# Optimization experiments

Hardware: AMD Instinct MI355X
Metric: run time of the kernel (lower is better)

Reference implementation:

```python
import jax, jax.numpy as jnp
import numpy as np

HIDDEN = 128
IN = 28
OUT = 28


def _uniform(key, shape, fan_in):
    bound = 1.0 / np.sqrt(fan_in)
    return jax.random.uniform(key, shape, jnp.float32, -bound, bound)


def setup_inputs() -> dict:
    key = jax.random.key(0)
    ks = jax.random.split(key, 8)
    B, T = 4096, 256
    x = jax.random.normal(ks[0], (B, T, IN), jnp.float32)
    hidden = jnp.zeros((B, HIDDEN), jnp.float32)
    # torch nn.Linear default init: U(-1/sqrt(fan_in), 1/sqrt(fan_in))
    W_ih = _uniform(ks[1], (HIDDEN, IN), IN)
    b_ih = _uniform(ks[2], (HIDDEN,), IN)
    W_hh = _uniform(ks[3], (HIDDEN, HIDDEN), HIDDEN)
    b_hh = _uniform(ks[4], (HIDDEN,), HIDDEN)
    W_ho = _uniform(ks[5], (OUT * OUT, HIDDEN), HIDDEN)
    b_ho = _uniform(ks[6], (OUT * OUT,), HIDDEN)
    return {"x": x, "hidden": hidden, "W_ih": W_ih, "b_ih": b_ih,
            "W_hh": W_hh, "b_hh": b_hh, "W_ho": W_ho, "b_ho": b_ho}


def reference(x, hidden, W_ih, b_ih, W_hh, b_hh, W_ho, b_ho):
    # x: [B, T, IN]; hidden: [B, HIDDEN]
    def step(h, x_t):
        h = jax.nn.relu(x_t @ W_ih.T + b_ih + h @ W_hh.T + b_hh)
        return h, None

    # scan over time (leading axis) — equivalent to the python loop,
    # and only the final hidden feeds the output projection (the torch
    # code overwrites `output` every step, so only the last one matters).
    h_final, _ = jax.lax.scan(step, hidden, jnp.swapaxes(x, 0, 1))
    out = (h_final @ W_ho.T + b_ho).reshape(-1, OUT, OUT)  # [B, 28, 28]
    return out, h_final
```

## Files before the change

kernel.cpp:

```cpp
#include <hip/hip_runtime.h>
#include <hip/hip_bf16.h>

#define B_TOT   4096
#define T_STEPS 256
#define IN_D    28
#define HID     128
#define OUT_D   784
#define BM      16

typedef __bf16 bf16x8 __attribute__((ext_vector_type(8)));
typedef __bf16 bf16x4 __attribute__((ext_vector_type(4)));
typedef float  f32x4  __attribute__((ext_vector_type(4)));
typedef float  f32x2  __attribute__((ext_vector_type(2)));

__device__ __forceinline__ float bf2f(__bf16 b) {
    unsigned short s = __builtin_bit_cast(unsigned short, b);
    unsigned int u = ((unsigned int)s) << 16;
    return __builtin_bit_cast(float, u);
}
__device__ __forceinline__ unsigned short f2bfbits(float f) {
    unsigned int u = __builtin_bit_cast(unsigned int, f);
    u += 0x7fffu + ((u >> 16) & 1u);
    return (unsigned short)(u >> 16);
}

__device__ __forceinline__ int hswz(int row, int byteInRow) {
    return row * 256 + (byteInRow ^ ((row & 7) << 4));
}

__global__ __launch_bounds__(256) void rnn_fused(
    const float* __restrict__ x,
    const float* __restrict__ h0,
    const float* __restrict__ W_ih,
    const float* __restrict__ b_ih,
    const float* __restrict__ W_hh,
    const float* __restrict__ b_hh,
    const float* __restrict__ W_ho,
    const float* __restrict__ b_ho,
    float* __restrict__ out)
{
    __shared__ __align__(16) unsigned char Hb[2][BM * 256];
    __shared__ __align__(16) unsigned char Xb[2][BM * 80];

    const int tid  = threadIdx.x;
    const int lane = tid & 63;
    const int wv   = tid >> 6;
    const int ln15 = lane & 15;
    const int lg   = lane >> 4;
    const int b0   = blockIdx.x * BM;

    const int nt0 = wv * 32;
    bf16x8 bw[2][4];
    #pragma unroll
    for (int ti = 0; ti < 2; ++ti) {
        int n = nt0 + ti * 16 + ln15;
        #pragma unroll
        for (int kc = 0; kc < 4; ++kc) {
            const float* p = W_hh + n * HID + kc * 32 + lg * 8;
            bf16x8 v;
            #pragma unroll
            for (int e = 0; e < 8; ++e) v[e] = (__bf16)p[e];
            bw[ti][kc] = v;
        }
    }
    const __bf16 bzero = (__bf16)0.0f;
    bf16x8 bxf[2];
    #pragma unroll
    for (int ti = 0; ti < 2; ++ti) {
        int n = nt0 + ti * 16 + ln15;
        bf16x8 v;
        #pragma unroll
        for (int e = 0; e < 8; ++e) {
            int k = lg * 8 + e;
            v[e] = (k < IN_D) ? (__bf16)W_ih[n * IN_D + k] : bzero;
        }
        bxf[ti] = v;
    }
    f32x4 bias4[2];
    #pragma unroll
    for (int ti = 0; ti < 2; ++ti) {
        int n = nt0 + ti * 16 + 4 * lg;
        f32x4 bi = *(const f32x4*)(b_ih + n);
        f32x4 bh = *(const f32x4*)(b_hh + n);
        bias4[ti] = bi + bh;
    }

    {
        int row = tid >> 4, cg = tid & 15;
        const float* p = h0 + (size_t)(b0 + row) * HID + cg * 8;
        bf16x8 hv;
        #pragma unroll
        for (int e = 0; e < 8; ++e) hv[e] = (__bf16)p[e];
        *(bf16x8*)(&Hb[0][hswz(row, cg * 16)]) = hv;
    }
    if (tid < 64) {
        int bufi = tid >> 5, idx = tid & 31, row = idx >> 1, half = idx & 1;
        *(unsigned int*)(&Xb[bufi][row * 80 + 56 + half * 4]) = 0u;
    }
    const int xrow = tid / 14, xpair = tid % 14;
    const bool xthr = (tid < 224);
    const float* xbase = x + (size_t)(b0 + xrow) * T_STEPS * IN_D + xpair * 2;
    if (xthr) {
        f32x2 v = *(const f32x2*)(xbase + 0 * IN_D);
        unsigned int pk = ((unsigned int)f2bfbits(v[1]) << 16) | f2bfbits(v[0]);
        *(unsigned int*)(&Xb[0][xrow * 80 + xpair * 4]) = pk;
    }
    f32x2 p0 = {0.f, 0.f}, p1 = p0, p2 = p0, p3 = p0;
    if (xthr) {
        p0 = *(const f32x2*)(xbase + 1 * IN_D);
        p1 = *(const f32x2*)(xbase + 2 * IN_D);
        p2 = *(const f32x2*)(xbase + 3 * IN_D);
        p3 = *(const f32x2*)(xbase + 4 * IN_D);
    }
    __syncthreads();

#define STEP(T, P)                                                              \
    {                                                                           \
        const int rb = (T) & 1;                                                 \
        bf16x8 ax  = *(const bf16x8*)(&Xb[rb][ln15 * 80 + lg * 16]);            \
        bf16x8 ah0 = *(const bf16x8*)(&Hb[rb][hswz(ln15,   0 + lg * 16)]);      \
        bf16x8 ah1 = *(const bf16x8*)(&Hb[rb][hswz(ln15,  64 + lg * 16)]);      \
        bf16x8 ah2 = *(const bf16x8*)(&Hb[rb][hswz(ln15, 128 + lg * 16)]);      \
        bf16x8 ah3 = *(const bf16x8*)(&Hb[rb][hswz(ln15, 192 + lg * 16)]);      \
        if (((T) + 1 < T_STEPS) && xthr) {                                      \
            unsigned int pk = ((unsigned int)f2bfbits(P[1]) << 16) | f2bfbits(P[0]); \
            *(unsigned int*)(&Xb[rb ^ 1][xrow * 80 + xpair * 4]) = pk;          \
        }                                                                       \
        if (((T) + 5 < T_STEPS) && xthr)                                        \
            P = *(const f32x2*)(xbase + (size_t)((T) + 5) * IN_D);              \
        f32x4 a0 = bias4[0], a1 = bias4[1];                                     \
        f32x4 c0 = {0.f, 0.f, 0.f, 0.f}, c1 = c0;                               \
        a0 = __builtin_amdgcn_mfma_f32_16x16x32_bf16(bxf[0],   ax,  a0, 0, 0, 0); \
        a1 = __builtin_amdgcn_mfma_f32_16x16x32_bf16(bxf[1],   ax,  a1, 0, 0, 0); \
        a0 = __builtin_amdgcn_mfma_f32_16x16x32_bf16(bw[0][0], ah0, a0, 0, 0, 0); \
        a1 = __builtin_amdgcn_mfma_f32_16x16x32_bf16(bw[1][0], ah0, a1, 0, 0, 0); \
        c0 = __builtin_amdgcn_mfma_f32_16x16x32_bf16(bw[0][1], ah1, c0, 0, 0, 0); \
        c1 = __builtin_amdgcn_mfma_f32_16x16x32_bf16(bw[1][1], ah1, c1, 0, 0, 0); \
        a0 = __builtin_amdgcn_mfma_f32_16x16x32_bf16(bw[0][2], ah2, a0, 0, 0, 0); \
        a1 = __builtin_amdgcn_mfma_f32_16x16x32_bf16(bw[1][2], ah2, a1, 0, 0, 0); \
        c0 = __builtin_amdgcn_mfma_f32_16x16x32_bf16(bw[0][3], ah3, c0, 0, 0, 0); \
        c1 = __builtin_amdgcn_mfma_f32_16x16x32_bf16(bw[1][3], ah3, c1, 0, 0, 0); \
        _Pragma("unroll")                                                       \
        for (int ti = 0; ti < 2; ++ti) {                                        \
            f32x4 s = ti ? (a1 + c1) : (a0 + c0);                               \
            bf16x4 w;                                                           \
            _Pragma("unroll")                                                   \
            for (int r = 0; r < 4; ++r) {                                       \
                float v = s[r];                                                 \
                w[r] = (__bf16)(v > 0.f ? v : 0.f);                             \
            }                                                                   \
            *(bf16x4*)(&Hb[rb ^ 1][hswz(ln15, nt0 * 2 + ti * 32 + lg * 8)]) = w; \
        }                                                                       \
        __syncthreads();                                                        \
    }

    for (int t = 0; t < T_STEPS; t += 4) {
        STEP(t + 0, p0)
        STEP(t + 1, p1)
        STEP(t + 2, p2)
        STEP(t + 3, p3)
    }
#undef STEP

    {
        int row = tid >> 4, cg = tid & 15;
        bf16x8 hv = *(const bf16x8*)(&Hb[0][hswz(row, cg * 16)]);
        float* po = out + (size_t)B_TOT * OUT_D + (size_t)(b0 + row) * HID + cg * 8;
        #pragma unroll
        for (int e = 0; e < 8; ++e) po[e] = bf2f(hv[e]);
    }
    bf16x8 af[4];
    #pragma unroll
    for (int kc = 0; kc < 4; ++kc)
        af[kc] = *(const bf16x8*)(&Hb[0][hswz(ln15, kc * 64 + lg * 16)]);

    for (int nt = wv; nt < 49; nt += 4) {
        f32x4 acc = *(const f32x4*)(b_ho + nt * 16 + 4 * lg);
        #pragma unroll
        for (int kc = 0; kc < 4; ++kc) {
            const float* p = W_ho + (nt * 16 + ln15) * HID + kc * 32 + lg * 8;
            bf16x8 bfrag;
            #pragma unroll
            for (int e = 0; e < 8; ++e) bfrag[e] = (__bf16)p[e];
            acc = __builtin_amdgcn_mfma_f32_16x16x32_bf16(bfrag, af[kc], acc, 0, 0, 0);
        }
        *(f32x4*)(out + (size_t)(b0 + ln15) * OUT_D + nt * 16 + 4 * lg) = acc;
    }
}

extern "C" void kernel_launch(void* const* d_in, const int* in_sizes, int n_in,
                              void* d_out, int out_size, void* d_ws, size_t ws_size,
                              hipStream_t stream) {
    const float* x    = (const float*)d_in[0];
    const float* h0   = (const float*)d_in[1];
    const float* W_ih = (const float*)d_in[2];
    const float* b_ih = (const float*)d_in[3];
    const float* W_hh = (const float*)d_in[4];
    const float* b_hh = (const float*)d_in[5];
    const float* W_ho = (const float*)d_in[6];
    const float* b_ho = (const float*)d_in[7];
    rnn_fused<<<B_TOT / BM, 256, 0, stream>>>(x, h0, W_ih, b_ih, W_hh, b_hh,
                                              W_ho, b_ho, (float*)d_out);
}
```

Measured before the change: 105.2 us.

## Load x fragments straight into registers and use an LDS-only barrier

Drops the shared-memory staging buffer for the input sequence. Each lane now loads its own MFMA x operand from global memory four steps ahead and converts it to bf16 in registers, so the per-step LDS write and read of x go away. Every wave issues its own x loads instead of sharing one staged copy, which adds redundant global loads. `__syncthreads` is replaced by a custom barrier that waits only on LDS counters, so outstanding global prefetches no longer stall the per-step barrier. This relies on the hand-written waitcnt being sufficient for correctness.

```diff
diff --git a/kernel.cpp b/kernel.cpp
--- a/kernel.cpp
+++ b/kernel.cpp
@@ -11,22 +11,18 @@
 typedef __bf16 bf16x8 __attribute__((ext_vector_type(8)));
 typedef __bf16 bf16x4 __attribute__((ext_vector_type(4)));
 typedef float  f32x4  __attribute__((ext_vector_type(4)));
-typedef float  f32x2  __attribute__((ext_vector_type(2)));
 
 __device__ __forceinline__ float bf2f(__bf16 b) {
     unsigned short s = __builtin_bit_cast(unsigned short, b);
     unsigned int u = ((unsigned int)s) << 16;
     return __builtin_bit_cast(float, u);
 }
-__device__ __forceinline__ unsigned short f2bfbits(float f) {
-    unsigned int u = __builtin_bit_cast(unsigned int, f);
-    u += 0x7fffu + ((u >> 16) & 1u);
-    return (unsigned short)(u >> 16);
-}
 
 __device__ __forceinline__ int hswz(int row, int byteInRow) {
     return row * 256 + (byteInRow ^ ((row & 7) << 4));
 }
+
+#define BAR() asm volatile("s_waitcnt lgkmcnt(0)\n\ts_barrier" ::: "memory")
 
 __global__ __launch_bounds__(256) void rnn_fused(
     const float* __restrict__ x,
@@ -40,7 +36,6 @@
     float* __restrict__ out)
 {
     __shared__ __align__(16) unsigned char Hb[2][BM * 256];
-    __shared__ __align__(16) unsigned char Xb[2][BM * 80];
 
     const int tid  = threadIdx.x;
     const int lane = tid & 63;
@@ -93,49 +88,37 @@
         for (int e = 0; e < 8; ++e) hv[e] = (__bf16)p[e];
         *(bf16x8*)(&Hb[0][hswz(row, cg * 16)]) = hv;
     }
-    if (tid < 64) {
-        int bufi = tid >> 5, idx = tid & 31, row = idx >> 1, half = idx & 1;
-        *(unsigned int*)(&Xb[bufi][row * 80 + 56 + half * 4]) = 0u;
-    }
-    const int xrow = tid / 14, xpair = tid % 14;
-    const bool xthr = (tid < 224);
-    const float* xbase = x + (size_t)(b0 + xrow) * T_STEPS * IN_D + xpair * 2;
-    if (xthr) {
-        f32x2 v = *(const f32x2*)(xbase + 0 * IN_D);
-        unsigned int pk = ((unsigned int)f2bfbits(v[1]) << 16) | f2bfbits(v[0]);
-        *(unsigned int*)(&Xb[0][xrow * 80 + xpair * 4]) = pk;
-    }
-    f32x2 p0 = {0.f, 0.f}, p1 = p0, p2 = p0, p3 = p0;
-    if (xthr) {
-        p0 = *(const f32x2*)(xbase + 1 * IN_D);
-        p1 = *(const f32x2*)(xbase + 2 * IN_D);
-        p2 = *(const f32x2*)(xbase + 3 * IN_D);
-        p3 = *(const f32x2*)(xbase + 4 * IN_D);
-    }
-    __syncthreads();
 
-#define STEP(T, P)                                                              \
+    const float* xlane  = x + (size_t)(b0 + ln15) * T_STEPS * IN_D + lg * 8;
+    const float* xlane2 = x + (size_t)(b0 + ln15) * T_STEPS * IN_D + (lg == 3 ? 24 : lg * 8 + 4);
+    f32x4 q0a = *(const f32x4*)(xlane  + 0 * IN_D), q0b = *(const f32x4*)(xlane2 + 0 * IN_D);
+    f32x4 q1a = *(const f32x4*)(xlane  + 1 * IN_D), q1b = *(const f32x4*)(xlane2 + 1 * IN_D);
+    f32x4 q2a = *(const f32x4*)(xlane  + 2 * IN_D), q2b = *(const f32x4*)(xlane2 + 2 * IN_D);
+    f32x4 q3a = *(const f32x4*)(xlane  + 3 * IN_D), q3b = *(const f32x4*)(xlane2 + 3 * IN_D);
+
+    BAR();
+
+#define STEP(T, QA, QB)                                                         \
     {                                                                           \
         const int rb = (T) & 1;                                                 \
-        bf16x8 ax  = *(const bf16x8*)(&Xb[rb][ln15 * 80 + lg * 16]);            \
         bf16x8 ah0 = *(const bf16x8*)(&Hb[rb][hswz(ln15,   0 + lg * 16)]);      \
         bf16x8 ah1 = *(const bf16x8*)(&Hb[rb][hswz(ln15,  64 + lg * 16)]);      \
         bf16x8 ah2 = *(const bf16x8*)(&Hb[rb][hswz(ln15, 128 + lg * 16)]);      \
         bf16x8 ah3 = *(const bf16x8*)(&Hb[rb][hswz(ln15, 192 + lg * 16)]);      \
-        if (((T) + 1 < T_STEPS) && xthr) {                                      \
-            unsigned int pk = ((unsigned int)f2bfbits(P[1]) << 16) | f2bfbits(P[0]); \
-            *(unsigned int*)(&Xb[rb ^ 1][xrow * 80 + xpair * 4]) = pk;          \
+        bf16x8 ax;                                                              \
+        _Pragma("unroll")                                                       \
+        for (int e = 0; e < 4; ++e) { ax[e] = (__bf16)QA[e]; ax[4 + e] = (__bf16)QB[e]; } \
+        f32x4 a0 = __builtin_amdgcn_mfma_f32_16x16x32_bf16(bxf[0], ax, bias4[0], 0, 0, 0); \
+        f32x4 a1 = __builtin_amdgcn_mfma_f32_16x16x32_bf16(bxf[1], ax, bias4[1], 0, 0, 0); \
+        if ((T) + 4 < T_STEPS) {                                                \
+            QA = *(const f32x4*)(xlane  + (size_t)((T) + 4) * IN_D);            \
+            QB = *(const f32x4*)(xlane2 + (size_t)((T) + 4) * IN_D);            \
         }                                                                       \
-        if (((T) + 5 < T_STEPS) && xthr)                                        \
-            P = *(const f32x2*)(xbase + (size_t)((T) + 5) * IN_D);              \
-        f32x4 a0 = bias4[0], a1 = bias4[1];                                     \
-        f32x4 c0 = {0.f, 0.f, 0.f, 0.f}, c1 = c0;                               \
-        a0 = __builtin_amdgcn_mfma_f32_16x16x32_bf16(bxf[0],   ax,  a0, 0, 0, 0); \
-        a1 = __builtin_amdgcn_mfma_f32_16x16x32_bf16(bxf[1],   ax,  a1, 0, 0, 0); \
+        f32x4 z = {0.f, 0.f, 0.f, 0.f};                                         \
         a0 = __builtin_amdgcn_mfma_f32_16x16x32_bf16(bw[0][0], ah0, a0, 0, 0, 0); \
         a1 = __builtin_amdgcn_mfma_f32_16x16x32_bf16(bw[1][0], ah0, a1, 0, 0, 0); \
-        c0 = __builtin_amdgcn_mfma_f32_16x16x32_bf16(bw[0][1], ah1, c0, 0, 0, 0); \
-        c1 = __builtin_amdgcn_mfma_f32_16x16x32_bf16(bw[1][1], ah1, c1, 0, 0, 0); \
+        f32x4 c0 = __builtin_amdgcn_mfma_f32_16x16x32_bf16(bw[0][1], ah1, z, 0, 0, 0); \
+        f32x4 c1 = __builtin_amdgcn_mfma_f32_16x16x32_bf16(bw[1][1], ah1, z, 0, 0, 0); \
         a0 = __builtin_amdgcn_mfma_f32_16x16x32_bf16(bw[0][2], ah2, a0, 0, 0, 0); \
         a1 = __builtin_amdgcn_mfma_f32_16x16x32_bf16(bw[1][2], ah2, a1, 0, 0, 0); \
         c0 = __builtin_amdgcn_mfma_f32_16x16x32_bf16(bw[0][3], ah3, c0, 0, 0, 0); \
@@ -151,14 +134,14 @@
             }                                                                   \
             *(bf16x4*)(&Hb[rb ^ 1][hswz(ln15, nt0 * 2 + ti * 32 + lg * 8)]) = w; \
         }                                                                       \
-        __syncthreads();                                                        \
+        BAR();                                                                  \
     }
 
     for (int t = 0; t < T_STEPS; t += 4) {
-        STEP(t + 0, p0)
-        STEP(t + 1, p1)
-        STEP(t + 2, p2)
-        STEP(t + 3, p3)
+        STEP(t + 0, q0a, q0b)
+        STEP(t + 1, q1a, q1b)
+        STEP(t + 2, q2a, q2b)
+        STEP(t + 3, q3a, q3b)
     }
 #undef STEP
 
```

After: 139.2 us. 1.32x slower.

## Stage x through an 8-slot LDS ring, batching four timesteps per load

Applied to the files above, without the earlier changes.

Replaces the two-slot x buffer, which was refilled every step from registers prefetched four steps ahead, with an 8-slot LDS ring. Every fourth step each thread loads four future timesteps of x, converts them to bf16 and writes them into the ring before that step's barrier. This cuts global-load and conversion work out of three of every four recurrent steps. The cost is that each batch is consumed within the same step it is issued, so global memory latency is no longer hidden behind several steps of compute and can stall the serial recurrence. It also folds the bias and zero accumulator initialisation directly into the first MFMAs.

```diff
diff --git a/kernel.cpp b/kernel.cpp
--- a/kernel.cpp
+++ b/kernel.cpp
@@ -40,7 +40,7 @@
     float* __restrict__ out)
 {
     __shared__ __align__(16) unsigned char Hb[2][BM * 256];
-    __shared__ __align__(16) unsigned char Xb[2][BM * 80];
+    __shared__ __align__(16) unsigned char Xs[8 * 1024];
 
     const int tid  = threadIdx.x;
     const int lane = tid & 63;
@@ -93,49 +93,40 @@
         for (int e = 0; e < 8; ++e) hv[e] = (__bf16)p[e];
         *(bf16x8*)(&Hb[0][hswz(row, cg * 16)]) = hv;
     }
-    if (tid < 64) {
-        int bufi = tid >> 5, idx = tid & 31, row = idx >> 1, half = idx & 1;
-        *(unsigned int*)(&Xb[bufi][row * 80 + 56 + half * 4]) = 0u;
+    {
+        int slot = tid >> 5, idx = tid & 31, row = idx >> 1, d = idx & 1;
+        *(unsigned int*)(&Xs[slot * 1024 + row * 64 + 56 + d * 4]) = 0u;
     }
     const int xrow = tid / 14, xpair = tid % 14;
     const bool xthr = (tid < 224);
     const float* xbase = x + (size_t)(b0 + xrow) * T_STEPS * IN_D + xpair * 2;
     if (xthr) {
-        f32x2 v = *(const f32x2*)(xbase + 0 * IN_D);
-        unsigned int pk = ((unsigned int)f2bfbits(v[1]) << 16) | f2bfbits(v[0]);
-        *(unsigned int*)(&Xb[0][xrow * 80 + xpair * 4]) = pk;
-    }
-    f32x2 p0 = {0.f, 0.f}, p1 = p0, p2 = p0, p3 = p0;
-    if (xthr) {
-        p0 = *(const f32x2*)(xbase + 1 * IN_D);
-        p1 = *(const f32x2*)(xbase + 2 * IN_D);
-        p2 = *(const f32x2*)(xbase + 3 * IN_D);
-        p3 = *(const f32x2*)(xbase + 4 * IN_D);
-    }
+        #pragma unroll
+        for (int s = 0; s < 4; ++s) {
+            f32x2 v = *(const f32x2*)(xbase + (size_t)s * IN_D);
+            unsigned int pk = ((unsigned int)f2bfbits(v[1]) << 16) | f2bfbits(v[0]);
+            *(unsigned int*)(&Xs[s * 1024 + xrow * 64 + xpair * 4]) = pk;
+        }
+    }
+    f32x2 sx0 = {0.f, 0.f}, sx1 = sx0, sx2 = sx0, sx3 = sx0;
     __syncthreads();
 
-#define STEP(T, P)                                                              \
+#define STEP(T, STGL, STGW)                                                     \
     {                                                                           \
         const int rb = (T) & 1;                                                 \
-        bf16x8 ax  = *(const bf16x8*)(&Xb[rb][ln15 * 80 + lg * 16]);            \
+        STGL                                                                    \
+        bf16x8 ax  = *(const bf16x8*)(&Xs[((T) & 7) * 1024 + ln15 * 64 + lg * 16]); \
         bf16x8 ah0 = *(const bf16x8*)(&Hb[rb][hswz(ln15,   0 + lg * 16)]);      \
         bf16x8 ah1 = *(const bf16x8*)(&Hb[rb][hswz(ln15,  64 + lg * 16)]);      \
         bf16x8 ah2 = *(const bf16x8*)(&Hb[rb][hswz(ln15, 128 + lg * 16)]);      \
         bf16x8 ah3 = *(const bf16x8*)(&Hb[rb][hswz(ln15, 192 + lg * 16)]);      \
-        if (((T) + 1 < T_STEPS) && xthr) {                                      \
-            unsigned int pk = ((unsigned int)f2bfbits(P[1]) << 16) | f2bfbits(P[0]); \
-            *(unsigned int*)(&Xb[rb ^ 1][xrow * 80 + xpair * 4]) = pk;          \
-        }                                                                       \
-        if (((T) + 5 < T_STEPS) && xthr)                                        \
-            P = *(const f32x2*)(xbase + (size_t)((T) + 5) * IN_D);              \
-        f32x4 a0 = bias4[0], a1 = bias4[1];                                     \
-        f32x4 c0 = {0.f, 0.f, 0.f, 0.f}, c1 = c0;                               \
-        a0 = __builtin_amdgcn_mfma_f32_16x16x32_bf16(bxf[0],   ax,  a0, 0, 0, 0); \
-        a1 = __builtin_amdgcn_mfma_f32_16x16x32_bf16(bxf[1],   ax,  a1, 0, 0, 0); \
+        f32x4 a0 = __builtin_amdgcn_mfma_f32_16x16x32_bf16(bxf[0], ax, bias4[0], 0, 0, 0); \
+        f32x4 a1 = __builtin_amdgcn_mfma_f32_16x16x32_bf16(bxf[1], ax, bias4[1], 0, 0, 0); \
+        f32x4 zz = {0.f, 0.f, 0.f, 0.f};                                        \
         a0 = __builtin_amdgcn_mfma_f32_16x16x32_bf16(bw[0][0], ah0, a0, 0, 0, 0); \
         a1 = __builtin_amdgcn_mfma_f32_16x16x32_bf16(bw[1][0], ah0, a1, 0, 0, 0); \
-        c0 = __builtin_amdgcn_mfma_f32_16x16x32_bf16(bw[0][1], ah1, c0, 0, 0, 0); \
-        c1 = __builtin_amdgcn_mfma_f32_16x16x32_bf16(bw[1][1], ah1, c1, 0, 0, 0); \
+        f32x4 c0 = __builtin_amdgcn_mfma_f32_16x16x32_bf16(bw[0][1], ah1, zz, 0, 0, 0); \
+        f32x4 c1 = __builtin_amdgcn_mfma_f32_16x16x32_bf16(bw[1][1], ah1, zz, 0, 0, 0); \
         a0 = __builtin_amdgcn_mfma_f32_16x16x32_bf16(bw[0][2], ah2, a0, 0, 0, 0); \
         a1 = __builtin_amdgcn_mfma_f32_16x16x32_bf16(bw[1][2], ah2, a1, 0, 0, 0); \
         c0 = __builtin_amdgcn_mfma_f32_16x16x32_bf16(bw[0][3], ah3, c0, 0, 0, 0); \
@@ -151,16 +142,42 @@
             }                                                                   \
             *(bf16x4*)(&Hb[rb ^ 1][hswz(ln15, nt0 * 2 + ti * 32 + lg * 8)]) = w; \
         }                                                                       \
+        STGW                                                                    \
         __syncthreads();                                                        \
     }
 
-    for (int t = 0; t < T_STEPS; t += 4) {
-        STEP(t + 0, p0)
-        STEP(t + 1, p1)
-        STEP(t + 2, p2)
-        STEP(t + 3, p3)
+#define STG_LOAD(T)                                                             \
+        if (((T) + 4 < T_STEPS) && xthr) {                                      \
+            sx0 = *(const f32x2*)(xbase + (size_t)((T) + 4) * IN_D);            \
+            sx1 = *(const f32x2*)(xbase + (size_t)((T) + 5) * IN_D);            \
+            sx2 = *(const f32x2*)(xbase + (size_t)((T) + 6) * IN_D);            \
+            sx3 = *(const f32x2*)(xbase + (size_t)((T) + 7) * IN_D);            \
+        }
+#define STG_WRITE(T)                                                            \
+        if (((T) + 4 < T_STEPS) && xthr) {                                      \
+            unsigned int p0 = ((unsigned int)f2bfbits(sx0[1]) << 16) | f2bfbits(sx0[0]); \
+            unsigned int p1 = ((unsigned int)f2bfbits(sx1[1]) << 16) | f2bfbits(sx1[0]); \
+            unsigned int p2 = ((unsigned int)f2bfbits(sx2[1]) << 16) | f2bfbits(sx2[0]); \
+            unsigned int p3 = ((unsigned int)f2bfbits(sx3[1]) << 16) | f2bfbits(sx3[0]); \
+            *(unsigned int*)(&Xs[(((T) + 4) & 7) * 1024 + xrow * 64 + xpair * 4]) = p0; \
+            *(unsigned int*)(&Xs[(((T) + 5) & 7) * 1024 + xrow * 64 + xpair * 4]) = p1; \
+            *(unsigned int*)(&Xs[(((T) + 6) & 7) * 1024 + xrow * 64 + xpair * 4]) = p2; \
+            *(unsigned int*)(&Xs[(((T) + 7) & 7) * 1024 + xrow * 64 + xpair * 4]) = p3; \
+        }
+
+    for (int t = 0; t < T_STEPS; t += 8) {
+        STEP(t + 0, STG_LOAD(t + 0), STG_WRITE(t + 0))
+        STEP(t + 1, , )
+        STEP(t + 2, , )
+        STEP(t + 3, , )
+        STEP(t + 4, STG_LOAD(t + 4), STG_WRITE(t + 4))
+        STEP(t + 5, , )
+        STEP(t + 6, , )
+        STEP(t + 7, , )
     }
 #undef STEP
+#undef STG_LOAD
+#undef STG_WRITE
 
     {
         int row = tid >> 4, cg = tid & 15;
```

Result: no change. 104.6 us (-0.6%).
